# Kernel optimization log

Measured on AMD Instinct MI355X. Metric: run time of the kernel, lower is better.

## Reference

```python
import jax, jax.numpy as jnp
import numpy as np

B, T, D, H = 4, 2048, 2048, 16
HD = D // H

def setup_inputs() -> dict:
    key = jax.random.key(0)
    k1, k2, k3 = jax.random.split(key, 3)
    x = jax.random.normal(k1, (B, T, D), dtype=jnp.float32)
    mask = jnp.ones((B, T), dtype=jnp.int32)
    # torch Linear weights, scaled like default init (~1/sqrt(fan_in))
    w_qkv = jax.random.normal(k2, (3 * D, D), dtype=jnp.float32) / np.sqrt(D)
    w_o = jax.random.normal(k3, (D, D), dtype=jnp.float32) / np.sqrt(D)
    return {"x": x, "mask": mask, "w_qkv": w_qkv, "w_o": w_o}

def reference(x, mask, w_qkv, w_o):
    # qkv projection: (B,T,D) @ (D,3D) -> (B,T,3D)
    qkv = jnp.einsum('btd,ed->bte', x, w_qkv)
    q, k, v = jnp.split(qkv, 3, axis=-1)
    # (B,T,D) -> (B,H,T,HD)
    def to_heads(t):
        return t.reshape(B, T, H, HD).transpose(0, 2, 1, 3)
    q, k, v = to_heads(q), to_heads(k), to_heads(v)
    scale = 1.0 / np.sqrt(HD).astype(np.float32)
    att = jnp.einsum('bhqd,bhkd->bhqk', q, k) * scale  # (B,H,T,T)
    att = jnp.where(mask[:, None, None, :] == 0, -jnp.inf, att)
    att = jax.nn.softmax(att, axis=-1)
    y = jnp.einsum('bhqk,bhkd->bhqd', att, v)  # (B,H,T,HD)
    y = y.transpose(0, 2, 1, 3).reshape(B, T, D)
    return jnp.einsum('btd,ed->bte', y, w_o)
```

## Files before the change

### kernel.cpp

```cpp
#include <hip/hip_runtime.h>
#include <hip/hip_bf16.h>

typedef __bf16 bf16;
typedef bf16 bf16x8 __attribute__((ext_vector_type(8)));
typedef float f32x4 __attribute__((ext_vector_type(4)));

struct alignas(8) bh4 { bf16 v[4]; };

__device__ __forceinline__ void glds16(const bf16* g, bf16* l) {
  __builtin_amdgcn_global_load_lds(
      (const __attribute__((address_space(1))) void*)g,
      (__attribute__((address_space(3))) void*)l, 16, 0, 0);
}

#define QSCALE (1.4426950408889634f / 11.313708498984761f)
#define DEFER_THR 8.0f

__global__ void convert_to_bf16(const float* __restrict__ s, bf16* __restrict__ dst,
                                long n) {
  const long stride = (long)gridDim.x * blockDim.x * 8;
  for (long i = ((long)blockIdx.x * blockDim.x + threadIdx.x) * 8; i < n; i += stride) {
    float4 a = *(const float4*)(s + i);
    float4 b = *(const float4*)(s + i + 4);
    bf16x8 o;
    o[0] = (bf16)a.x; o[1] = (bf16)a.y; o[2] = (bf16)a.z; o[3] = (bf16)a.w;
    o[4] = (bf16)b.x; o[5] = (bf16)b.y; o[6] = (bf16)b.z; o[7] = (bf16)b.w;
    *(bf16x8*)(dst + i) = o;
  }
}

template <int MODE>
__global__ __launch_bounds__(512, 2)
void gemm256(const bf16* __restrict__ A, const bf16* __restrict__ Bw,
             void* __restrict__ C0v, bf16* __restrict__ C1,
             bf16* __restrict__ C2, int M, int N, int K) {
  __shared__ __align__(16) bf16 sA[2][2][128 * 64];
  __shared__ __align__(16) bf16 sB[2][2][128 * 64];
  const int tid = threadIdx.x;
  const int lane = tid & 63;
  const int wid = tid >> 6;
  const int wm = wid >> 2, wn = wid & 3;
  const int quad = lane >> 4, l16 = lane & 15;

  const int gx = gridDim.x;
  const int nwg = gx * gridDim.y;
  const int bid0 = blockIdx.y * gx + blockIdx.x;
  const int cpx = nwg >> 3;
  const int bid = (bid0 & 7) * cpx + (bid0 >> 3);
  const int bm = (bid / gx) * 256, bn = (bid % gx) * 256;

  f32x4 acc[8][4] = {};

  const int s_r = tid >> 3;
  const int s_cs = ((tid & 7) ^ (s_r & 7)) * 8;
  const int grB0 = ((s_r >> 5) << 6) + (s_r & 31);

  auto stageA = [&](int bufi, int hh, int ktile) {
    const int k0 = ktile << 6;
    bf16* dst = &sA[bufi][hh][0] + tid * 8;
    const bf16* src = A + (size_t)(bm + hh * 64 + s_r) * K + k0 + s_cs;
    glds16(src, dst);
    glds16(src + (size_t)128 * K, dst + 4096);
  };
  auto stageB = [&](int bufi, int hh, int ktile) {
    const int k0 = ktile << 6;
    bf16* dst = &sB[bufi][hh][0] + tid * 8;
    const bf16* src = Bw + (size_t)(bn + hh * 32 + grB0) * K + k0 + s_cs;
    glds16(src, dst);
    glds16(src + (size_t)128 * K, dst + 4096);
  };

  const int NT = K >> 6;
  stageA(0, 0, 0);
  stageB(0, 0, 0);
  stageB(0, 1, 0);
  stageA(0, 1, 0);
  stageA(1, 0, 1);
  stageB(1, 0, 1);
  stageB(1, 1, 1);
  asm volatile("s_waitcnt vmcnt(6)" ::: "memory");
  __builtin_amdgcn_s_barrier();

  for (int kt = 0; kt < NT; ++kt) {
    const int buf = kt & 1;
    bf16x8 af[4][2], bfA[2][2], bfB[2][2];

#pragma unroll
    for (int mt = 0; mt < 4; ++mt) {
      const int lr = wm * 64 + mt * 16 + l16;
#pragma unroll
      for (int s = 0; s < 2; ++s)
        af[mt][s] = *(const bf16x8*)&sA[buf][0][lr * 64 + (((s * 4 + quad) ^ (lr & 7)) * 8)];
    }
#pragma unroll
    for (int nt = 0; nt < 2; ++nt) {
      const int lr = wn * 32 + nt * 16 + l16;
#pragma unroll
      for (int s = 0; s < 2; ++s)
        bfA[nt][s] = *(const bf16x8*)&sB[buf][0][lr * 64 + (((s * 4 + quad) ^ (lr & 7)) * 8)];
    }
    if (kt + 1 < NT) stageA(buf ^ 1, 1, kt + 1);
    __builtin_amdgcn_s_barrier();
    asm volatile("s_waitcnt lgkmcnt(0)" ::: "memory");
    __builtin_amdgcn_sched_barrier(0);
    __builtin_amdgcn_s_setprio(1);
#pragma unroll
    for (int mt = 0; mt < 4; ++mt)
#pragma unroll
      for (int nt = 0; nt < 2; ++nt)
#pragma unroll
        for (int s = 0; s < 2; ++s)
          acc[mt][nt] = __builtin_amdgcn_mfma_f32_16x16x32_bf16(af[mt][s], bfA[nt][s], acc[mt][nt], 0, 0, 0);
    __builtin_amdgcn_s_setprio(0);
    __builtin_amdgcn_s_barrier();

#pragma unroll
    for (int nt = 0; nt < 2; ++nt) {
      const int lr = wn * 32 + nt * 16 + l16;
#pragma unroll
      for (int s = 0; s < 2; ++s)
        bfB[nt][s] = *(const bf16x8*)&sB[buf][1][lr * 64 + (((s * 4 + quad) ^ (lr & 7)) * 8)];
    }
    if (kt + 2 < NT) stageA(buf, 0, kt + 2);
    __builtin_amdgcn_s_barrier();
    asm volatile("s_waitcnt lgkmcnt(0)" ::: "memory");
    __builtin_amdgcn_sched_barrier(0);
    __builtin_amdgcn_s_setprio(1);
#pragma unroll
    for (int mt = 0; mt < 4; ++mt)
#pragma unroll
      for (int nt = 0; nt < 2; ++nt)
#pragma unroll
        for (int s = 0; s < 2; ++s)
          acc[mt][2 + nt] = __builtin_amdgcn_mfma_f32_16x16x32_bf16(af[mt][s], bfB[nt][s], acc[mt][2 + nt], 0, 0, 0);
    __builtin_amdgcn_s_setprio(0);
    __builtin_amdgcn_s_barrier();

#pragma unroll
    for (int mt = 0; mt < 4; ++mt) {
      const int lr = wm * 64 + mt * 16 + l16;
#pragma unroll
      for (int s = 0; s < 2; ++s)
        af[mt][s] = *(const bf16x8*)&sA[buf][1][lr * 64 + (((s * 4 + quad) ^ (lr & 7)) * 8)];
    }
    if (kt + 2 < NT) stageB(buf, 0, kt + 2);
    __builtin_amdgcn_s_barrier();
    asm volatile("s_waitcnt lgkmcnt(0)" ::: "memory");
    __builtin_amdgcn_sched_barrier(0);
    __builtin_amdgcn_s_setprio(1);
#pragma unroll
    for (int mt = 0; mt < 4; ++mt)
#pragma unroll
      for (int nt = 0; nt < 2; ++nt)
#pragma unroll
        for (int s = 0; s < 2; ++s)
          acc[4 + mt][nt] = __builtin_amdgcn_mfma_f32_16x16x32_bf16(af[mt][s], bfA[nt][s], acc[4 + mt][nt], 0, 0, 0);
    __builtin_amdgcn_s_setprio(0);
    __builtin_amdgcn_s_barrier();

    if (kt + 2 < NT) stageB(buf, 1, kt + 2);
    __builtin_amdgcn_s_barrier();
    __builtin_amdgcn_s_setprio(1);
#pragma unroll
    for (int mt = 0; mt < 4; ++mt)
#pragma unroll
      for (int nt = 0; nt < 2; ++nt)
#pragma unroll
        for (int s = 0; s < 2; ++s)
          acc[4 + mt][2 + nt] = __builtin_amdgcn_mfma_f32_16x16x32_bf16(af[mt][s], bfB[nt][s], acc[4 + mt][2 + nt], 0, 0, 0);
    __builtin_amdgcn_s_setprio(0);
    if (kt < NT - 1) {
      if (kt < NT - 2) asm volatile("s_waitcnt vmcnt(6)" ::: "memory");
      else             asm volatile("s_waitcnt vmcnt(0)" ::: "memory");
      __builtin_amdgcn_s_barrier();
    }
  }

  if (MODE == 0) {
    bf16* C0 = (bf16*)C0v;
#pragma unroll
    for (int i = 0; i < 8; ++i) {
      const int m0 = bm + wm * 128 + i * 16 + quad * 4;
      const int b = m0 >> 11, t0 = m0 & 2047;
#pragma unroll
      for (int j = 0; j < 4; ++j) {
        const int ncol = bn + wn * 64 + j * 16 + l16;
        const int which = ncol >> 11;
        const int d = ncol & 2047;
        const int h = d >> 7, hd = d & 127;
        if (which == 0) {
          bf16* dst = C0 + (((size_t)(b * 16 + h) * 2048 + t0) * 128 + hd);
#pragma unroll
          for (int r = 0; r < 4; ++r) dst[(size_t)r * 128] = (bf16)(acc[i][j][r] * QSCALE);
        } else if (which == 1) {
          bf16* dst = C1 + (((size_t)(b * 16 + h) * 2048 + t0) * 128 + hd);
#pragma unroll
          for (int r = 0; r < 4; ++r) dst[(size_t)r * 128] = (bf16)acc[i][j][r];
        } else {
          bh4 pk;
#pragma unroll
          for (int r = 0; r < 4; ++r) pk.v[r] = (bf16)acc[i][j][r];
          *(bh4*)(C2 + ((size_t)((b * 16 + h) * 128 + hd) * 2048 + t0)) = pk;
        }
      }
    }
  } else {
    float* C0 = (float*)C0v;
#pragma unroll
    for (int i = 0; i < 8; ++i) {
      const int m0 = bm + wm * 128 + i * 16 + quad * 4;
#pragma unroll
      for (int j = 0; j < 4; ++j) {
        const int n = bn + wn * 64 + j * 16 + l16;
#pragma unroll
        for (int r = 0; r < 4; ++r)
          C0[(size_t)(m0 + r) * N + n] = acc[i][j][r];
      }
    }
  }
}

__global__ __launch_bounds__(256, 3)
void attn_kernel(const bf16* __restrict__ Q, const bf16* __restrict__ Kb,
                 const bf16* __restrict__ Vt, const int* __restrict__ mask,
                 bf16* __restrict__ Y) {
  __shared__ __align__(16) bf16 smem[25600];
  bf16* sK = smem;
  bf16* sV = smem + 8192;
  bf16* sP = smem + 16384;

  const int tid = threadIdx.x;
  const int lane = tid & 63, w = tid >> 6;
  const int quad = lane >> 4, l16 = lane & 15;
  const int bh = blockIdx.x, b = bh >> 4, h = bh & 15;
  const int qt = blockIdx.y;
  const size_t head = (size_t)bh * (2048 * 128);

  bf16x8 qf[2][4];
#pragma unroll
  for (int nt = 0; nt < 2; ++nt) {
    const int t = qt * 128 + w * 32 + nt * 16 + l16;
    const bf16* g = Q + head + (size_t)t * 128 + quad * 8;
#pragma unroll
    for (int kk = 0; kk < 4; ++kk)
      qf[nt][kk] = *(const bf16x8*)(g + kk * 32);
  }

  f32x4 o[8][2] = {};
  float mrow[2] = {-3.0e38f, -3.0e38f};
  float lrow[2] = {0.0f, 0.0f};

  const int* maskb = mask + b * 2048;
  bf16* sPw = sP + w * (32 * 72);

  unsigned long long vmask;
  {
    const int4* mp4 = (const int4*)maskb;
    bool ok = true;
#pragma unroll
    for (int j = 0; j < 8; ++j) {
      const int4 q4 = mp4[lane * 8 + j];
      ok = ok && (q4.x != 0) && (q4.y != 0) && (q4.z != 0) && (q4.w != 0);
    }
    vmask = __ballot(ok);
  }

  for (int kt = 0; kt < 32; ++kt) {
    const int key0 = kt * 64;
    {
      const int cp = lane & 15;
      const int rbase = w * 16 + (lane >> 4);
#pragma unroll
      for (int p = 0; p < 4; ++p) {
        const int row = rbase + p * 4;
        const int c = (cp & 8) | ((cp ^ row) & 7);
        glds16(Kb + head + (size_t)(key0 + row) * 128 + c * 8,
               &sK[(w * 16 + p * 4) * 128 + lane * 8]);
      }
    }
    {
      const int cp = lane & 7;
      const int rbase = w * 32 + (lane >> 3);
#pragma unroll
      for (int p = 0; p < 4; ++p) {
        const int row = rbase + p * 8;
        const int c = cp ^ (row & 7);
        glds16(Vt + head + (size_t)row * 2048 + key0 + c * 8,
               &sV[(w * 32 + p * 8) * 64 + lane * 8]);
      }
    }
    __syncthreads();

    f32x4 st[4][2] = {};
#pragma unroll
    for (int kk = 0; kk < 4; ++kk) {
      bf16x8 ak[4];
#pragma unroll
      for (int mt = 0; mt < 4; ++mt) {
        const int row = mt * 16 + l16;
        const int c = kk * 4 + quad;
        const int cp = (c & 8) | ((c ^ row) & 7);
        ak[mt] = *(const bf16x8*)&sK[row * 128 + cp * 8];
      }
#pragma unroll
      for (int mt = 0; mt < 4; ++mt)
#pragma unroll
        for (int nt = 0; nt < 2; ++nt)
          st[mt][nt] = __builtin_amdgcn_mfma_f32_16x16x32_bf16(ak[mt], qf[nt][kk], st[mt][nt], 0, 0, 0);
    }

    if (((vmask >> (2 * kt)) & 3ULL) != 3ULL) {
#pragma unroll
      for (int mt = 0; mt < 4; ++mt) {
#pragma unroll
        for (int r = 0; r < 4; ++r) {
          const int mk = maskb[key0 + mt * 16 + quad * 4 + r];
#pragma unroll
          for (int nt = 0; nt < 2; ++nt)
            if (mk == 0) { st[mt][nt][r] = -1.0e30f; }
        }
      }
    }

#pragma unroll
    for (int nt = 0; nt < 2; ++nt) {
      float mx = -1.0e30f;
#pragma unroll
      for (int mt = 0; mt < 4; ++mt)
#pragma unroll
        for (int r = 0; r < 4; ++r) mx = fmaxf(mx, st[mt][nt][r]);
      mx = fmaxf(mx, __shfl_xor(mx, 16));
      mx = fmaxf(mx, __shfl_xor(mx, 32));
      if (!__all(mx <= mrow[nt] + DEFER_THR)) {
        const float newm = fmaxf(mrow[nt], mx);
        const float alpha = exp2f(mrow[nt] - newm);
        mrow[nt] = newm;
        lrow[nt] *= alpha;
#pragma unroll
        for (int mt = 0; mt < 8; ++mt)
#pragma unroll
          for (int r = 0; r < 4; ++r) o[mt][nt][r] *= alpha;
      }
      const float m = mrow[nt];
      float rs = 0.0f;
#pragma unroll
      for (int mt = 0; mt < 4; ++mt) {
        bh4 pk;
#pragma unroll
        for (int r = 0; r < 4; ++r) {
          const float p = exp2f(st[mt][nt][r] - m);
          rs += p;
          pk.v[r] = (bf16)p;
        }
        *(bh4*)&sPw[(nt * 16 + l16) * 72 + mt * 16 + quad * 4] = pk;
      }
      rs += __shfl_xor(rs, 16);
      rs += __shfl_xor(rs, 32);
      lrow[nt] += rs;
    }

#pragma unroll
    for (int kk = 0; kk < 2; ++kk) {
      bf16x8 bp[2];
#pragma unroll
      for (int nt = 0; nt < 2; ++nt)
        bp[nt] = *(const bf16x8*)&sPw[(nt * 16 + l16) * 72 + kk * 32 + quad * 8];
#pragma unroll
      for (int mt = 0; mt < 8; ++mt) {
        const int row = mt * 16 + l16;
        const int c = kk * 4 + quad;
        bf16x8 av = *(const bf16x8*)&sV[row * 64 + (c ^ (row & 7)) * 8];
#pragma unroll
        for (int nt = 0; nt < 2; ++nt)
          o[mt][nt] = __builtin_amdgcn_mfma_f32_16x16x32_bf16(av, bp[nt], o[mt][nt], 0, 0, 0);
      }
    }
    __syncthreads();
  }

  bf16* sOw = smem + w * 4352;
#pragma unroll
  for (int nt = 0; nt < 2; ++nt) {
    const float inv = 1.0f / lrow[nt];
#pragma unroll
    for (int mt = 0; mt < 8; ++mt) {
      bh4 pk;
#pragma unroll
      for (int r = 0; r < 4; ++r) pk.v[r] = (bf16)(o[mt][nt][r] * inv);
      *(bh4*)&sOw[(nt * 16 + l16) * 136 + mt * 16 + quad * 4] = pk;
    }
  }
  {
    const int col = (lane & 15) * 8;
#pragma unroll
    for (int p = 0; p < 8; ++p) {
      const int row = p * 4 + (lane >> 4);
      int4 v = *(const int4*)&sOw[row * 136 + col];
      const int token = qt * 128 + w * 32 + row;
      *(int4*)(Y + ((size_t)(b * 2048 + token)) * 2048 + h * 128 + col) = v;
    }
  }
}

extern "C" void kernel_launch(void* const* d_in, const int* in_sizes, int n_in,
                              void* d_out, int out_size, void* d_ws, size_t ws_size,
                              hipStream_t stream) {
  const float* x_raw  = (const float*)d_in[0];
  const int*   mask   = (const int*)d_in[1];
  const float* wq_raw = (const float*)d_in[2];
  const float* wo_raw = (const float*)d_in[3];
  float* out = (float*)d_out;

  char* ws = (char*)d_ws;
  const size_t MB = 1024 * 1024;
  bf16* xb  = (bf16*)(ws + 256);
  bf16* wqb = (bf16*)(ws + 256 + 32 * MB);
  bf16* qb  = (bf16*)(ws + 256 + 56 * MB);
  bf16* kb  = (bf16*)(ws + 256 + 88 * MB);
  bf16* vt  = (bf16*)(ws + 256 + 120 * MB);
  bf16* yb  = xb;
  bf16* wob = wqb;

  convert_to_bf16<<<1024, 256, 0, stream>>>(x_raw, xb, (long)in_sizes[0]);
  convert_to_bf16<<<1024, 256, 0, stream>>>(wq_raw, wqb, (long)in_sizes[2]);

  gemm256<0><<<dim3(24, 32), 512, 0, stream>>>(xb, wqb, qb, kb, vt, 8192, 6144, 2048);

  convert_to_bf16<<<1024, 256, 0, stream>>>(wo_raw, wob, (long)in_sizes[3]);

  attn_kernel<<<dim3(64, 16), 256, 0, stream>>>(qb, kb, vt, mask, yb);

  gemm256<1><<<dim3(8, 32), 512, 0, stream>>>(yb, wob, out, nullptr, nullptr, 8192, 2048, 2048);
}
```

Measured before the change: 606.5 us.

## Prefetch next K/V tiles into LDS while computing current tile

Restructures the attention loop so that the next K tile is loaded once QK^T finishes and the next V tile once PV finishes. Full __syncthreads are replaced by explicit vmcnt/lgkmcnt waits and barriers. This overlaps global-to-LDS copies with softmax and MFMA work instead of stalling at the top of each iteration. It also changes the P buffer stride from 72 to 76 to cut LDS bank conflicts, which needs two 8-byte reads instead of one 16-byte read. The counted waits are fragile, since the vmcnt values must match the exact number of outstanding loads.

```diff
diff --git a/kernel.cpp b/kernel.cpp
--- a/kernel.cpp
+++ b/kernel.cpp
@@ -2,6 +2,7 @@
 #include <hip/hip_bf16.h>
 
 typedef __bf16 bf16;
+typedef bf16 bf16x4 __attribute__((ext_vector_type(4)));
 typedef bf16 bf16x8 __attribute__((ext_vector_type(8)));
 typedef float f32x4 __attribute__((ext_vector_type(4)));
 
@@ -224,7 +225,7 @@
 void attn_kernel(const bf16* __restrict__ Q, const bf16* __restrict__ Kb,
                  const bf16* __restrict__ Vt, const int* __restrict__ mask,
                  bf16* __restrict__ Y) {
-  __shared__ __align__(16) bf16 smem[25600];
+  __shared__ __align__(16) bf16 smem[26112];
   bf16* sK = smem;
   bf16* sV = smem + 8192;
   bf16* sP = smem + 16384;
@@ -251,7 +252,7 @@
   float lrow[2] = {0.0f, 0.0f};
 
   const int* maskb = mask + b * 2048;
-  bf16* sPw = sP + w * (32 * 72);
+  bf16* sPw = sP + w * (32 * 76);
 
   unsigned long long vmask;
   {
@@ -265,31 +266,36 @@
     vmask = __ballot(ok);
   }
 
+  const int cpK = lane & 15, rbK = w * 16 + (lane >> 4);
+  const int cpV = lane & 7,  rbV = w * 32 + (lane >> 3);
+  auto stageK = [&](int kt2) {
+    const int key0 = kt2 * 64;
+#pragma unroll
+    for (int p = 0; p < 4; ++p) {
+      const int row = rbK + p * 4;
+      const int c = (cpK & 8) | ((cpK ^ row) & 7);
+      glds16(Kb + head + (size_t)(key0 + row) * 128 + c * 8,
+             &sK[(w * 16 + p * 4) * 128 + lane * 8]);
+    }
+  };
+  auto stageV = [&](int kt2) {
+    const int key0 = kt2 * 64;
+#pragma unroll
+    for (int p = 0; p < 4; ++p) {
+      const int row = rbV + p * 8;
+      const int c = cpV ^ (row & 7);
+      glds16(Vt + head + (size_t)row * 2048 + key0 + c * 8,
+             &sV[(w * 32 + p * 8) * 64 + lane * 8]);
+    }
+  };
+
+  stageK(0);
+  stageV(0);
+
   for (int kt = 0; kt < 32; ++kt) {
     const int key0 = kt * 64;
-    {
-      const int cp = lane & 15;
-      const int rbase = w * 16 + (lane >> 4);
-#pragma unroll
-      for (int p = 0; p < 4; ++p) {
-        const int row = rbase + p * 4;
-        const int c = (cp & 8) | ((cp ^ row) & 7);
-        glds16(Kb + head + (size_t)(key0 + row) * 128 + c * 8,
-               &sK[(w * 16 + p * 4) * 128 + lane * 8]);
-      }
-    }
-    {
-      const int cp = lane & 7;
-      const int rbase = w * 32 + (lane >> 3);
-#pragma unroll
-      for (int p = 0; p < 4; ++p) {
-        const int row = rbase + p * 8;
-        const int c = cp ^ (row & 7);
-        glds16(Vt + head + (size_t)row * 2048 + key0 + c * 8,
-               &sV[(w * 32 + p * 8) * 64 + lane * 8]);
-      }
-    }
-    __syncthreads();
+    asm volatile("s_waitcnt vmcnt(4)" ::: "memory");
+    __builtin_amdgcn_s_barrier();
 
     f32x4 st[4][2] = {};
 #pragma unroll
@@ -308,6 +314,9 @@
         for (int nt = 0; nt < 2; ++nt)
           st[mt][nt] = __builtin_amdgcn_mfma_f32_16x16x32_bf16(ak[mt], qf[nt][kk], st[mt][nt], 0, 0, 0);
     }
+    asm volatile("s_waitcnt lgkmcnt(0)" ::: "memory");
+    __builtin_amdgcn_s_barrier();
+    if (kt + 1 < 32) stageK(kt + 1);
 
     if (((vmask >> (2 * kt)) & 3ULL) != 3ULL) {
 #pragma unroll
@@ -352,19 +361,27 @@
           rs += p;
           pk.v[r] = (bf16)p;
         }
-        *(bh4*)&sPw[(nt * 16 + l16) * 72 + mt * 16 + quad * 4] = pk;
+        *(bh4*)&sPw[(nt * 16 + l16) * 76 + mt * 16 + quad * 4] = pk;
       }
       rs += __shfl_xor(rs, 16);
       rs += __shfl_xor(rs, 32);
       lrow[nt] += rs;
     }
 
+    if (kt + 1 < 32) asm volatile("s_waitcnt vmcnt(4)" ::: "memory");
+    else             asm volatile("s_waitcnt vmcnt(0)" ::: "memory");
+    __builtin_amdgcn_s_barrier();
+
 #pragma unroll
     for (int kk = 0; kk < 2; ++kk) {
       bf16x8 bp[2];
 #pragma unroll
-      for (int nt = 0; nt < 2; ++nt)
-        bp[nt] = *(const bf16x8*)&sPw[(nt * 16 + l16) * 72 + kk * 32 + quad * 8];
+      for (int nt = 0; nt < 2; ++nt) {
+        const int base = (nt * 16 + l16) * 76 + kk * 32 + quad * 8;
+        bf16x4 p0 = *(const bf16x4*)&sPw[base];
+        bf16x4 p1 = *(const bf16x4*)&sPw[base + 4];
+        bp[nt] = __builtin_shufflevector(p0, p1, 0, 1, 2, 3, 4, 5, 6, 7);
+      }
 #pragma unroll
       for (int mt = 0; mt < 8; ++mt) {
         const int row = mt * 16 + l16;
@@ -375,7 +392,9 @@
           o[mt][nt] = __builtin_amdgcn_mfma_f32_16x16x32_bf16(av, bp[nt], o[mt][nt], 0, 0, 0);
       }
     }
-    __syncthreads();
+    asm volatile("s_waitcnt lgkmcnt(0)" ::: "memory");
+    __builtin_amdgcn_s_barrier();
+    if (kt + 1 < 32) stageV(kt + 1);
   }
 
   bf16* sOw = smem + w * 4352;
```

After: 643.7 us. 1.06x slower.
